# Kernel optimization log

Measured on AMD Instinct MI355X. Metric: run time of the kernel, lower is better.

## Reference

```python
import jax, jax.numpy as jnp
import numpy as np

N_VERTICES = 24  # hardcoded via torch.eye(24) in the original
K = 3


def normalized_adj(adj):
    # scipy version: L = (A @ D^-1/2).T @ D^-1/2 = D^-1/2 @ A^T @ D^-1/2
    d = adj.sum(axis=1)
    d_inv_sqrt = jnp.where(d > 0, 1.0 / jnp.sqrt(d), 0.0)
    return (adj * d_inv_sqrt[None, :]).T * d_inv_sqrt[None, :]


def cheb_polynomials(L, k_order):
    Ts = [jnp.eye(N_VERTICES, dtype=L.dtype), L]
    for _ in range(2, k_order):
        Ts.append(2.0 * L @ Ts[-1] - Ts[-2])
    return jnp.stack(Ts[:k_order])  # (K, N, N)


def setup_inputs() -> dict:
    key = jax.random.key(0)
    k1, k2, k3 = jax.random.split(key, 3)
    x = jax.random.normal(k1, (64, 32, N_VERTICES, 512), dtype=jnp.float32)
    adj = jax.random.uniform(k2, (N_VERTICES, N_VERTICES), dtype=jnp.float32)
    Theta = jax.random.normal(k3, (K, 32, 32), dtype=jnp.float32)
    return {"x": x, "adj": adj, "Theta": Theta}


def reference(x, adj, Theta):
    # x: (b, c, n, t); adj: (n, n); Theta: (K, c, o)
    L = normalized_adj(adj)
    T = cheb_polynomials(L, K)  # (K, n, m)
    # original per-timestep, per-k: rhs[b,m,c] = sum_n x[b,n,c] T_k[n,m];
    # out[b,m,o] += rhs @ Theta_k. Fused over t and k, final permute -> (b,o,m,t).
    out = jnp.einsum('knm,bcnt,kco->bomt', T, x, Theta)
    return out
```

## Files before the change

kernel.cpp:

```cpp
#include <hip/hip_runtime.h>
#include <stdint.h>


#define NV 24
#define CIN 32
#define COUT 32
#define TDIM 512
#define BATCH 64
#define MDIM 768
#define KD 768
#define BM 128
#define BN 128
#define BK 32

typedef __attribute__((ext_vector_type(8))) short short8v;
typedef __attribute__((ext_vector_type(4))) float float4v;

__device__ inline unsigned short f2bf(float f) {
    unsigned int u = __float_as_uint(f);
    unsigned int r = (u + 0x7fffu + ((u >> 16) & 1u)) >> 16;
    return (unsigned short)r;
}

__global__ __launch_bounds__(256) void prep_w(const float* __restrict__ adj,
                                              const float* __restrict__ Theta,
                                              unsigned short* __restrict__ W) {
    __shared__ float adjS[NV * NV];
    __shared__ float disS[NV];
    __shared__ float LS[NV * NV];
    __shared__ float T2S[NV * NV];
    int tid = threadIdx.x;
    for (int e = tid; e < NV * NV; e += 256) adjS[e] = adj[e];
    __syncthreads();
    if (tid < NV) {
        float d = 0.f;
        for (int j = 0; j < NV; ++j) d += adjS[tid * NV + j];
        disS[tid] = (d > 0.f) ? rsqrtf(d) : 0.f;
    }
    __syncthreads();
    for (int e = tid; e < NV * NV; e += 256) {
        int i = e / NV, j = e % NV;
        LS[e] = disS[i] * adjS[j * NV + i] * disS[j];
    }
    __syncthreads();
    for (int e = tid; e < NV * NV; e += 256) {
        int i = e / NV, j = e % NV;
        float s = 0.f;
        for (int p = 0; p < NV; ++p) s += LS[i * NV + p] * LS[p * NV + j];
        T2S[e] = 2.f * s - (i == j ? 1.f : 0.f);
    }
    __syncthreads();
    int r0 = blockIdx.x * (MDIM / 64);
    for (int e = tid; e < (MDIM / 64) * KD; e += 256) {
        int lr = e / KD, col = e % KD;
        int row = r0 + lr;
        int o = row / NV, m = row % NV;
        int c = col / NV, n = col % NV;
        float th0 = Theta[0 * CIN * COUT + c * COUT + o];
        float th1 = Theta[1 * CIN * COUT + c * COUT + o];
        float th2 = Theta[2 * CIN * COUT + c * COUT + o];
        float v = (n == m ? th0 : 0.f) + LS[n * NV + m] * th1 + T2S[n * NV + m] * th2;
        W[(size_t)row * KD + col] = f2bf(v);
    }
}

__global__ __launch_bounds__(256) void convert_xT(const float* __restrict__ x,
                                                  unsigned short* __restrict__ xT) {
    __shared__ float tile[64][65];
    int b = blockIdx.y;
    int cnTile = blockIdx.x % 12;
    int tTile = blockIdx.x / 12;
    int tid = threadIdx.x;
    int cg = tid & 15;
    int rr = tid >> 4;
    const float* xb = x + (size_t)b * KD * TDIM + (size_t)(cnTile * 64) * TDIM + tTile * 64;
#pragma unroll
    for (int p = 0; p < 4; ++p) {
        int r = p * 16 + rr;
        float4 v = *(const float4*)(xb + (size_t)r * TDIM + cg * 4);
        tile[r][cg * 4 + 0] = v.x;
        tile[r][cg * 4 + 1] = v.y;
        tile[r][cg * 4 + 2] = v.z;
        tile[r][cg * 4 + 3] = v.w;
    }
    __syncthreads();
    unsigned short* dst = xT + (size_t)b * TDIM * KD + (size_t)(tTile * 64) * KD + cnTile * 64;
#pragma unroll
    for (int p = 0; p < 4; ++p) {
        int t = p * 16 + rr;
        ushort4 pk;
        pk.x = f2bf(tile[cg * 4 + 0][t]);
        pk.y = f2bf(tile[cg * 4 + 1][t]);
        pk.z = f2bf(tile[cg * 4 + 2][t]);
        pk.w = f2bf(tile[cg * 4 + 3][t]);
        *(ushort4*)(dst + (size_t)t * KD + cg * 4) = pk;
    }
}

__global__ __launch_bounds__(256) void gemm_cheb(const unsigned short* __restrict__ W,
                                                 const unsigned short* __restrict__ xT,
                                                 float* __restrict__ out) {
    __shared__ __attribute__((aligned(16))) unsigned short As[BM * BK];
    __shared__ __attribute__((aligned(16))) unsigned short Bs[BN * BK];
    int b = blockIdx.y;
    int mtile = blockIdx.x % 6;
    int ntile = blockIdx.x / 6;
    int tid = threadIdx.x;
    int wave = tid >> 6;
    int lane = tid & 63;
    int quad = lane >> 4;
    int l16 = lane & 15;
    int wm = wave >> 1, wn = wave & 1;

    const unsigned short* gA = W + (size_t)(mtile * BM) * KD;
    const unsigned short* gB = xT + (size_t)b * TDIM * KD + (size_t)(ntile * BN) * KD;

    int lrow = lane >> 2;
    int lchunk = lane & 3;
    int s0 = wave * 2;

    const float4v zero4 = {0.f, 0.f, 0.f, 0.f};
    float4v acc[4][4];
#pragma unroll
    for (int i = 0; i < 4; ++i)
#pragma unroll
        for (int j = 0; j < 4; ++j) acc[i][j] = zero4;

    for (int kt = 0; kt < KD / BK; ++kt) {
        __syncthreads();
        int k0 = kt * BK;
#pragma unroll
        for (int j = 0; j < 2; ++j) {
            int s = s0 + j;
            int row = s * 16 + lrow;
            const unsigned short* srcA = gA + (size_t)row * KD + k0 + lchunk * 8;
            const unsigned short* srcB = gB + (size_t)row * KD + k0 + lchunk * 8;
            __builtin_amdgcn_global_load_lds(
                (const __attribute__((address_space(1))) void*)srcA,
                (__attribute__((address_space(3))) void*)(As + s * 512), 16, 0, 0);
            __builtin_amdgcn_global_load_lds(
                (const __attribute__((address_space(1))) void*)srcB,
                (__attribute__((address_space(3))) void*)(Bs + s * 512), 16, 0, 0);
        }
        __syncthreads();
        short8v a[4], bb[4];
#pragma unroll
        for (int i = 0; i < 4; ++i)
            a[i] = *(const short8v*)(As + (wm * 64 + i * 16 + l16) * BK + quad * 8);
#pragma unroll
        for (int j = 0; j < 4; ++j)
            bb[j] = *(const short8v*)(Bs + (wn * 64 + j * 16 + l16) * BK + quad * 8);
#pragma unroll
        for (int i = 0; i < 4; ++i)
#pragma unroll
            for (int j = 0; j < 4; ++j)
                acc[i][j] = __builtin_amdgcn_mfma_f32_16x16x32_bf16(a[i], bb[j], acc[i][j], 0, 0, 0);
    }

    float* outB = out + (size_t)b * MDIM * TDIM;
    int rbase = mtile * BM + wm * 64;
    int cbase = ntile * BN + wn * 64;
#pragma unroll
    for (int i = 0; i < 4; ++i) {
#pragma unroll
        for (int j = 0; j < 4; ++j) {
            int row0 = rbase + i * 16 + quad * 4;
            int col = cbase + j * 16 + l16;
#pragma unroll
            for (int r = 0; r < 4; ++r)
                outB[(size_t)(row0 + r) * TDIM + col] = acc[i][j][r];
        }
    }
}

extern "C" void kernel_launch(void* const* d_in, const int* in_sizes, int n_in,
                              void* d_out, int out_size, void* d_ws, size_t ws_size,
                              hipStream_t stream) {
    const float* x = (const float*)d_in[0];
    const float* adj = (const float*)d_in[1];
    const float* Theta = (const float*)d_in[2];
    float* out = (float*)d_out;

    unsigned short* xT = (unsigned short*)d_ws;
    unsigned short* W = (unsigned short*)((char*)d_ws + (size_t)BATCH * TDIM * KD * 2);

    prep_w<<<64, 256, 0, stream>>>(adj, Theta, W);
    convert_xT<<<dim3(12 * 8, BATCH), 256, 0, stream>>>(x, xT);
    gemm_cheb<<<dim3(6 * 4, BATCH), 256, 0, stream>>>(W, xT, out);
}
```

Before: 252.6 us.

## Pre-pack W and x into contiguous per-k-tile blobs for GEMM loads

Both GEMM operands are now written in a tile-packed layout in which each 128x32 k-slice is one contiguous 8 KB block. The GEMM's global-to-LDS loads then read fully linear memory instead of strided 64-byte row segments, which should improve coalescing and DRAM efficiency. The transpose kernel changes its tiling to produce this layout, which alters its read pattern and LDS usage.

```diff
diff --git a/kernel.cpp b/kernel.cpp
--- a/kernel.cpp
+++ b/kernel.cpp
@@ -12,6 +12,10 @@
 #define BM 128
 #define BN 128
 #define BK 32
+#define NKT (KD / BK)
+#define NTT (TDIM / BN)
+#define NMT (MDIM / BM)
+#define BLOB (BM * BK)
 
 typedef __attribute__((ext_vector_type(8))) short short8v;
 typedef __attribute__((ext_vector_type(4))) float float4v;
@@ -24,7 +28,7 @@
 
 __global__ __launch_bounds__(256) void prep_w(const float* __restrict__ adj,
                                               const float* __restrict__ Theta,
-                                              unsigned short* __restrict__ W) {
+                                              unsigned short* __restrict__ Wp) {
     __shared__ float adjS[NV * NV];
     __shared__ float disS[NV];
     __shared__ float LS[NV * NV];
@@ -60,51 +64,52 @@
         float th1 = Theta[1 * CIN * COUT + c * COUT + o];
         float th2 = Theta[2 * CIN * COUT + c * COUT + o];
         float v = (n == m ? th0 : 0.f) + LS[n * NV + m] * th1 + T2S[n * NV + m] * th2;
-        W[(size_t)row * KD + col] = f2bf(v);
+        size_t idx = (((size_t)(row >> 7) * NKT + (col >> 5)) * BM + (row & 127)) * BK + (col & 31);
+        Wp[idx] = f2bf(v);
     }
 }
 
-__global__ __launch_bounds__(256) void convert_xT(const float* __restrict__ x,
-                                                  unsigned short* __restrict__ xT) {
-    __shared__ float tile[64][65];
+__global__ __launch_bounds__(256) void convert_xP(const float* __restrict__ x,
+                                                  unsigned short* __restrict__ xP) {
+    __shared__ float tile[BK][133];
+    int kt = blockIdx.x % NKT;
+    int tt = blockIdx.x / NKT;
     int b = blockIdx.y;
-    int cnTile = blockIdx.x % 12;
-    int tTile = blockIdx.x / 12;
     int tid = threadIdx.x;
-    int cg = tid & 15;
-    int rr = tid >> 4;
-    const float* xb = x + (size_t)b * KD * TDIM + (size_t)(cnTile * 64) * TDIM + tTile * 64;
+    const float* src = x + (size_t)b * KD * TDIM + (size_t)(kt * BK) * TDIM + tt * BN;
 #pragma unroll
     for (int p = 0; p < 4; ++p) {
-        int r = p * 16 + rr;
-        float4 v = *(const float4*)(xb + (size_t)r * TDIM + cg * 4);
-        tile[r][cg * 4 + 0] = v.x;
-        tile[r][cg * 4 + 1] = v.y;
-        tile[r][cg * 4 + 2] = v.z;
-        tile[r][cg * 4 + 3] = v.w;
+        int e = p * 256 + tid;
+        int r = e >> 5, c4 = e & 31;
+        float4 v = *(const float4*)(src + (size_t)r * TDIM + c4 * 4);
+        tile[r][c4 * 4 + 0] = v.x;
+        tile[r][c4 * 4 + 1] = v.y;
+        tile[r][c4 * 4 + 2] = v.z;
+        tile[r][c4 * 4 + 3] = v.w;
     }
     __syncthreads();
-    unsigned short* dst = xT + (size_t)b * TDIM * KD + (size_t)(tTile * 64) * KD + cnTile * 64;
+    unsigned short* dst = xP + ((size_t)(b * NTT + tt) * NKT + kt) * BLOB;
+    int kq = tid & 7, tb = tid >> 3;
 #pragma unroll
     for (int p = 0; p < 4; ++p) {
-        int t = p * 16 + rr;
+        int t = p * 32 + tb;
         ushort4 pk;
-        pk.x = f2bf(tile[cg * 4 + 0][t]);
-        pk.y = f2bf(tile[cg * 4 + 1][t]);
-        pk.z = f2bf(tile[cg * 4 + 2][t]);
-        pk.w = f2bf(tile[cg * 4 + 3][t]);
-        *(ushort4*)(dst + (size_t)t * KD + cg * 4) = pk;
+        pk.x = f2bf(tile[kq * 4 + 0][t]);
+        pk.y = f2bf(tile[kq * 4 + 1][t]);
+        pk.z = f2bf(tile[kq * 4 + 2][t]);
+        pk.w = f2bf(tile[kq * 4 + 3][t]);
+        *(ushort4*)(dst + t * BK + kq * 4) = pk;
     }
 }
 
-__global__ __launch_bounds__(256) void gemm_cheb(const unsigned short* __restrict__ W,
-                                                 const unsigned short* __restrict__ xT,
+__global__ __launch_bounds__(256) void gemm_cheb(const unsigned short* __restrict__ Wp,
+                                                 const unsigned short* __restrict__ xP,
                                                  float* __restrict__ out) {
-    __shared__ __attribute__((aligned(16))) unsigned short As[BM * BK];
-    __shared__ __attribute__((aligned(16))) unsigned short Bs[BN * BK];
+    __shared__ __attribute__((aligned(16))) unsigned short As[BLOB];
+    __shared__ __attribute__((aligned(16))) unsigned short Bs[BLOB];
     int b = blockIdx.y;
-    int mtile = blockIdx.x % 6;
-    int ntile = blockIdx.x / 6;
+    int mt = blockIdx.x % NMT;
+    int tt = blockIdx.x / NMT;
     int tid = threadIdx.x;
     int wave = tid >> 6;
     int lane = tid & 63;
@@ -112,12 +117,8 @@
     int l16 = lane & 15;
     int wm = wave >> 1, wn = wave & 1;
 
-    const unsigned short* gA = W + (size_t)(mtile * BM) * KD;
-    const unsigned short* gB = xT + (size_t)b * TDIM * KD + (size_t)(ntile * BN) * KD;
-
-    int lrow = lane >> 2;
-    int lchunk = lane & 3;
-    int s0 = wave * 2;
+    const unsigned short* Ab = Wp + (size_t)mt * NKT * BLOB;
+    const unsigned short* Bb = xP + (size_t)(b * NTT + tt) * NKT * BLOB;
 
     const float4v zero4 = {0.f, 0.f, 0.f, 0.f};
     float4v acc[4][4];
@@ -126,21 +127,22 @@
 #pragma unroll
         for (int j = 0; j < 4; ++j) acc[i][j] = zero4;
 
-    for (int kt = 0; kt < KD / BK; ++kt) {
+    for (int kt = 0; kt < NKT; ++kt) {
         __syncthreads();
-        int k0 = kt * BK;
+        const unsigned short* abase = Ab + (size_t)kt * BLOB;
+        const unsigned short* bbase = Bb + (size_t)kt * BLOB;
 #pragma unroll
-        for (int j = 0; j < 2; ++j) {
-            int s = s0 + j;
-            int row = s * 16 + lrow;
-            const unsigned short* srcA = gA + (size_t)row * KD + k0 + lchunk * 8;
-            const unsigned short* srcB = gB + (size_t)row * KD + k0 + lchunk * 8;
+        for (int h = 0; h < 2; ++h) {
+            const unsigned short* sa = abase + (h * 256 + tid) * 8;
+            const unsigned short* sb = bbase + (h * 256 + tid) * 8;
+            unsigned short* da = As + (h * 256 + wave * 64) * 8;
+            unsigned short* db = Bs + (h * 256 + wave * 64) * 8;
             __builtin_amdgcn_global_load_lds(
-                (const __attribute__((address_space(1))) void*)srcA,
-                (__attribute__((address_space(3))) void*)(As + s * 512), 16, 0, 0);
+                (const __attribute__((address_space(1))) void*)sa,
+                (__attribute__((address_space(3))) void*)da, 16, 0, 0);
             __builtin_amdgcn_global_load_lds(
-                (const __attribute__((address_space(1))) void*)srcB,
-                (__attribute__((address_space(3))) void*)(Bs + s * 512), 16, 0, 0);
+                (const __attribute__((address_space(1))) void*)sb,
+                (__attribute__((address_space(3))) void*)db, 16, 0, 0);
         }
         __syncthreads();
         short8v a[4], bb[4];
@@ -158,8 +160,8 @@
     }
 
     float* outB = out + (size_t)b * MDIM * TDIM;
-    int rbase = mtile * BM + wm * 64;
-    int cbase = ntile * BN + wn * 64;
+    int rbase = mt * BM + wm * 64;
+    int cbase = tt * BN + wn * 64;
 #pragma unroll
     for (int i = 0; i < 4; ++i) {
 #pragma unroll
@@ -181,10 +183,10 @@
     const float* Theta = (const float*)d_in[2];
     float* out = (float*)d_out;
 
-    unsigned short* xT = (unsigned short*)d_ws;
-    unsigned short* W = (unsigned short*)((char*)d_ws + (size_t)BATCH * TDIM * KD * 2);
+    unsigned short* xP = (unsigned short*)d_ws;
+    unsigned short* Wp = (unsigned short*)((char*)d_ws + (size_t)BATCH * TDIM * KD * 2);
 
-    prep_w<<<64, 256, 0, stream>>>(adj, Theta, W);
-    convert_xT<<<dim3(12 * 8, BATCH), 256, 0, stream>>>(x, xT);
-    gemm_cheb<<<dim3(6 * 4, BATCH), 256, 0, stream>>>(W, xT, out);
+    prep_w<<<64, 256, 0, stream>>>(adj, Theta, Wp);
+    convert_xP<<<dim3(NKT * NTT, BATCH), 256, 0, stream>>>(x, xP);
+    gemm_cheb<<<dim3(NMT * NTT, BATCH), 256, 0, stream>>>(Wp, xP, out);
 }
```

After: 245.3 us. -2.9%, faster.
